# Kernel optimization log

Hardware: AMD Instinct MI355X
Metric: run time of the kernel (lower is better)

## Reference

```python
import jax, jax.numpy as jnp
import numpy as np


def setup_inputs() -> dict:
    key = jax.random.key(0)
    k1, k2, k3, k4 = jax.random.split(key, 4)
    N, C, T, V = 32, 64, 300, 25
    x = jax.random.normal(k1, (N, C, T, V), dtype=jnp.float32)
    # xavier_uniform-like scale for W (gain=1.414), small normal for alpha/phi
    xavier_scale = 1.414 * (2.0 / (C + C)) ** 0.5
    W = jax.random.normal(k2, (C, C), dtype=jnp.float32) * xavier_scale
    alpha = jax.random.normal(k3, (C // 4, C), dtype=jnp.float32) * 0.1
    phi = jax.random.normal(k4, (C // 4, C), dtype=jnp.float32) * 0.1
    return {"x": x, "W": W, "alpha": alpha, "phi": phi, "kernel": 9, "stride": 2}


def reference(x, W, alpha, phi, kernel, stride):
    N, C, T, V = x.shape
    # [N, C, T, V] -> [N*V, T, C]
    xv = jnp.transpose(x, (0, 3, 2, 1)).reshape(N * V, T, C)
    xw = xv @ W  # [NV, T, C]
    x1 = jnp.einsum('hc,ntc->nth', alpha, xw)  # [NV, T, H]
    x2 = jnp.einsum('hc,ntc->nth', phi, xw)    # [NV, T, H]
    scores = jnp.einsum('nth,nsh->nts', x1, x2)  # [NV, T, T]
    # banded local-window mask I: row i keeps cols |i-j| <= kernel//2 (multiplicative,
    # NOT -inf masking -- faithful to the original torch.mul before softmax)
    idx = jnp.arange(T)
    band = (jnp.abs(idx[:, None] - idx[None, :]) <= kernel // 2).astype(xw.dtype)
    masked = scores * band
    # one-hot selection matmul W_sel @ masked == strided row gather at 0, stride, 2*stride, ...
    sel_rows = jnp.arange(0, T, stride)  # length ceil(T/stride)
    sel = masked[:, sel_rows, :]  # [NV, T', T]
    attn = jax.nn.softmax(sel, axis=-1)
    out = jnp.einsum('nts,nsc->ntc', attn, xw)  # [NV, T', C]
    Tp = out.shape[1]
    # [NV, T', C] -> [N, C, T', V]
    return jnp.transpose(out.reshape(N, V, Tp, C), (0, 3, 2, 1))
```

## Files before the change

kernel.cpp:

```cpp
#include <hip/hip_runtime.h>

#define NB 32
#define CC 64
#define CS 32
#define TT 300
#define VV 25
#define HH 16
#define TPOUT 150
#define KH 4
#define TC 4
#define TPG 5

#define ALD 72
#define FLD 100

typedef __attribute__((ext_vector_type(4))) float f32x4;
typedef __attribute__((ext_vector_type(8))) short bf16x8;

static __device__ __forceinline__ unsigned short f2bf(float f) {
    unsigned u = __float_as_uint(f);
    unsigned r = (u + 0x7FFFu + ((u >> 16) & 1u)) >> 16;
    return (unsigned short)r;
}
static __device__ __forceinline__ float bf2f(unsigned short h) {
    return __uint_as_float(((unsigned)h) << 16);
}
static __device__ __forceinline__ float bfLO(unsigned u) {
    return __uint_as_float(u << 16);
}
static __device__ __forceinline__ float bfHI(unsigned u) {
    return __uint_as_float(u & 0xffff0000u);
}

__global__ __launch_bounds__(256) void k0_prep(const float* __restrict__ W,
                                               const float* __restrict__ alpha,
                                               const float* __restrict__ phi,
                                               unsigned short* __restrict__ Wh,
                                               unsigned short* __restrict__ Wl,
                                               float* __restrict__ ssum) {
    const int tid = threadIdx.x;
    {
        int i = blockIdx.x * 256 + tid;
        if (i < 12800)
            reinterpret_cast<float4*>(ssum)[i] = (float4){0.f, 0.f, 0.f, 0.f};
    }
    if (blockIdx.x != 0) return;

    __shared__ float sW[64][64];
    __shared__ float sA[32][64];
    __shared__ float sWe[64][96];
    for (int i = tid; i < 1024; i += 256)
        reinterpret_cast<float4*>(&sW[0][0])[i] = reinterpret_cast<const float4*>(W)[i];
    for (int i = tid; i < 512; i += 256) {
        float4 v = (i < 256) ? reinterpret_cast<const float4*>(alpha)[i]
                             : reinterpret_cast<const float4*>(phi)[i - 256];
        reinterpret_cast<float4*>(&sA[0][0])[i] = v;
    }
    __syncthreads();
    for (int i = tid; i < 1024; i += 256) {
        int ci = i >> 4, q = i & 15;
        *reinterpret_cast<float4*>(&sWe[ci][4 * q]) =
            reinterpret_cast<const float4*>(&sW[ci][0])[q];
    }
    for (int i = tid; i < 2048; i += 256) {
        int ci = i >> 5, j = i & 31;
        const float4* a = reinterpret_cast<const float4*>(&sW[ci][0]);
        const float4* b = reinterpret_cast<const float4*>(&sA[j][0]);
        float acc = 0.f;
#pragma unroll
        for (int q = 0; q < 16; ++q) {
            float4 u = a[q], w = b[q];
            acc += u.x * w.x + u.y * w.y + u.z * w.z + u.w * w.w;
        }
        sWe[ci][64 + j] = acc;
    }
    __syncthreads();
    for (int i = tid; i < 6144; i += 256) {
        int k = i / 96, c = i - 96 * k;
        float f = sWe[k][c];
        unsigned short h = f2bf(f);
        int off = (((k >> 3) * 96) + c) * 8 + (k & 7);
        Wh[off] = h;
        Wl[off] = f2bf(f - bf2f(h));
    }
}

__global__ __launch_bounds__(512) void k1_mfma(const float* __restrict__ x,
                                               const unsigned short* __restrict__ Bh,
                                               const unsigned short* __restrict__ Bl,
                                               unsigned short* __restrict__ xwv,
                                               float* __restrict__ xws,
                                               float* __restrict__ ssum) {
    __shared__ __align__(16) char smem[40000];
    unsigned short (*sAh)[ALD] = reinterpret_cast<unsigned short(*)[ALD]>(smem);
    unsigned short (*sAl)[ALD] = reinterpret_cast<unsigned short(*)[ALD]>(smem + 18432);
    float (*sF)[FLD] = reinterpret_cast<float(*)[FLD]>(smem);

    const int n  = blockIdx.y;
    const int t0 = blockIdx.x * TC;
    const int tid = threadIdx.x;

    if (tid < 400) {
        const int cig = tid & 15, tq = tid >> 4;
        const float* xp = x + (size_t)n * CC * TT * VV + (size_t)t0 * VV + 4 * tq;
        unsigned short mh[4][4], ml[4][4];
#pragma unroll
        for (int u = 0; u < 4; ++u) {
            const int ci = cig * 4 + u;
            float4 v = *reinterpret_cast<const float4*>(&xp[(size_t)ci * TT * VV]);
            unsigned short h0 = f2bf(v.x), h1 = f2bf(v.y), h2 = f2bf(v.z), h3 = f2bf(v.w);
            mh[0][u] = h0; mh[1][u] = h1; mh[2][u] = h2; mh[3][u] = h3;
            ml[0][u] = f2bf(v.x - bf2f(h0));
            ml[1][u] = f2bf(v.y - bf2f(h1));
            ml[2][u] = f2bf(v.z - bf2f(h2));
            ml[3][u] = f2bf(v.w - bf2f(h3));
        }
#pragma unroll
        for (int i = 0; i < 4; ++i) {
            *reinterpret_cast<uint2*>(&sAh[4 * tq + i][cig * 4]) =
                *reinterpret_cast<const uint2*>(&mh[i][0]);
            *reinterpret_cast<uint2*>(&sAl[4 * tq + i][cig * 4]) =
                *reinterpret_cast<const uint2*>(&ml[i][0]);
        }
    }
    __syncthreads();

    const int w    = tid >> 6;
    const int lane = tid & 63;
    const int lm   = lane & 15;
    const int g    = lane >> 4;
    const int mc   = w * 16 + lm;

    f32x4 acc[6];
#pragma unroll
    for (int b = 0; b < 6; ++b) acc[b] = (f32x4){0.f, 0.f, 0.f, 0.f};

#pragma unroll
    for (int kh = 0; kh < 2; ++kh) {
        const int kb = kh * 32 + g * 8;
        const int kc = kb >> 3;
        bf16x8 ah = *reinterpret_cast<const bf16x8*>(&sAh[mc][kb]);
        bf16x8 al = *reinterpret_cast<const bf16x8*>(&sAl[mc][kb]);
#pragma unroll
        for (int nt = 0; nt < 6; ++nt) {
            const int nc = nt * 16 + lm;
            bf16x8 bh = *reinterpret_cast<const bf16x8*>(&Bh[(size_t)(kc * 96 + nc) * 8]);
            acc[nt] = __builtin_amdgcn_mfma_f32_16x16x32_bf16(ah, bh, acc[nt], 0, 0, 0);
            if (nt >= 4) {
                bf16x8 bl = *reinterpret_cast<const bf16x8*>(&Bl[(size_t)(kc * 96 + nc) * 8]);
                acc[nt] = __builtin_amdgcn_mfma_f32_16x16x32_bf16(ah, bl, acc[nt], 0, 0, 0);
                acc[nt] = __builtin_amdgcn_mfma_f32_16x16x32_bf16(al, bh, acc[nt], 0, 0, 0);
            }
        }
    }
    __syncthreads();

#pragma unroll
    for (int j = 0; j < 4; ++j) {
        const int row = w * 16 + g * 4 + j;
        if (row < 100) {
#pragma unroll
            for (int nt = 0; nt < 6; ++nt)
                sF[row][nt * 16 + lm] = acc[nt][j];
        }
    }
    __syncthreads();

    for (int i = tid; i < 1600; i += 512) {
        const int vv = i >> 6, c = i & 63;
        float s = sF[vv][c] + sF[vv + 25][c] + sF[vv + 50][c] + sF[vv + 75][c];
        atomicAdd(&ssum[((size_t)n * VV + vv) * CC + c], s);
    }
    for (int i = tid; i < 1600; i += 512) {
        const int row = i >> 4, q = i & 15;
        const int tloc = row / 25, vv = row - 25 * tloc;
        size_t dst = (((size_t)n * VV + vv) * TT + (t0 + tloc)) * CC + 4 * q;
        float4 v = *reinterpret_cast<const float4*>(&sF[row][4 * q]);
        ushort4 b = {f2bf(v.x), f2bf(v.y), f2bf(v.z), f2bf(v.w)};
        *reinterpret_cast<ushort4*>(&xwv[dst]) = b;
    }
    for (int i = tid; i < 800; i += 512) {
        const int row = i >> 3, q = i & 7;
        const int tloc = row / 25, vv = row - 25 * tloc;
        size_t dst = (((size_t)n * VV + vv) * TT + (t0 + tloc)) * CS + 4 * q;
        *reinterpret_cast<float4*>(&xws[dst]) =
            *reinterpret_cast<const float4*>(&sF[row][64 + 4 * q]);
    }
}

__global__ __launch_bounds__(512) void k2_fused(const unsigned short* __restrict__ xwv,
                                                const float* __restrict__ xws,
                                                const float* __restrict__ ssum,
                                                float* __restrict__ out) {
    const int tpg = blockIdx.x;
    const int n   = blockIdx.y;
    const int tid = threadIdx.x;
    const int tp0 = tpg * TPG;

    __shared__ float sOut[TPG * VV][65];
    __shared__ float sss[VV][CC];
    __shared__ float sscore[TPG][VV][9];
    __shared__ float scoef[TPG][VV][10];

    for (int i = tid; i < VV * CC; i += 512)
        (&sss[0][0])[i] = ssum[((size_t)n * VV) * CC + i];

    for (int j = tid; j < TPG * VV * 9; j += 512) {
        const int tpl = j / (VV * 9);
        const int rem = j - tpl * (VV * 9);
        const int v = rem / 9, k = rem - 9 * v;
        const int t = 2 * (tp0 + tpl);
        const int s = t - KH + k;
        float sc = 0.f;
        if (s >= 0 && s < TT) {
            const size_t r = (size_t)n * VV + v;
            const float4* x1 = reinterpret_cast<const float4*>(&xws[(r * TT + t) * CS]);
            const float4* x2 = reinterpret_cast<const float4*>(&xws[(r * TT + s) * CS + 16]);
#pragma unroll
            for (int q = 0; q < 4; ++q) {
                float4 a = x1[q], b = x2[q];
                sc += a.x * b.x + a.y * b.y + a.z * b.z + a.w * b.w;
            }
        }
        sscore[tpl][v][k] = sc;
    }
    __syncthreads();

    for (int j = tid; j < TPG * VV; j += 512) {
        const int tpl = j / VV, v = j - tpl * VV;
        const int t = 2 * (tp0 + tpl);
        float m = 0.f;
        int nb = 0;
#pragma unroll
        for (int k = 0; k < 9; ++k) {
            int s = t - KH + k;
            if (s >= 0 && s < TT) { nb++; m = fmaxf(m, sscore[tpl][v][k]); }
        }
        float wbg = __expf(-m);
        float Z = (float)(TT - nb) * wbg;
        float e[9];
#pragma unroll
        for (int k = 0; k < 9; ++k) {
            int s = t - KH + k;
            float ek = (s >= 0 && s < TT) ? __expf(sscore[tpl][v][k] - m) : 0.f;
            e[k] = ek;
            Z += ek;
        }
        float inv = 1.f / Z;
#pragma unroll
        for (int k = 0; k < 9; ++k) {
            int s = t - KH + k;
            scoef[tpl][v][k] = (s >= 0 && s < TT) ? (e[k] - wbg) * inv : 0.f;
        }
        scoef[tpl][v][9] = wbg * inv;
    }
    __syncthreads();

    for (int j = tid; j < TPG * VV * 8; j += 512) {
        const int w  = j >> 3;
        const int cg = j & 7;
        const int tpl = w / VV, v = w - tpl * VV;
        const int t = 2 * (tp0 + tpl);
        const size_t rbase = ((size_t)n * VV + v) * TT;
        const int c0 = cg * 8;

        float val[8];
        {
            const float cbg = scoef[tpl][v][9];
#pragma unroll
            for (int i = 0; i < 8; ++i) val[i] = cbg * sss[v][c0 + i];
        }
#pragma unroll
        for (int k = 0; k < 9; ++k) {
            int s = t - KH + k;
            s = min(max(s, 0), TT - 1);
            const float cf = scoef[tpl][v][k];
            uint4 u = *reinterpret_cast<const uint4*>(&xwv[(rbase + s) * CC + c0]);
            val[0] = fmaf(cf, bfLO(u.x), val[0]);
            val[1] = fmaf(cf, bfHI(u.x), val[1]);
            val[2] = fmaf(cf, bfLO(u.y), val[2]);
            val[3] = fmaf(cf, bfHI(u.y), val[3]);
            val[4] = fmaf(cf, bfLO(u.z), val[4]);
            val[5] = fmaf(cf, bfHI(u.z), val[5]);
            val[6] = fmaf(cf, bfLO(u.w), val[6]);
            val[7] = fmaf(cf, bfHI(u.w), val[7]);
        }
#pragma unroll
        for (int i = 0; i < 8; ++i) sOut[w][c0 + i] = val[i];
    }
    __syncthreads();

    float* dst = out + ((size_t)n * CC * TPOUT * VV + (size_t)tp0 * VV);
    for (int j = tid; j < CC * TPG * VV; j += 512) {
        const int c = j / (TPG * VV);
        const int w = j - c * (TPG * VV);
        dst[(size_t)c * (TPOUT * VV) + w] = sOut[w][c];
    }
}

extern "C" void kernel_launch(void* const* d_in, const int* in_sizes, int n_in,
                              void* d_out, int out_size, void* d_ws, size_t ws_size,
                              hipStream_t stream) {
    const float* x     = (const float*)d_in[0];
    const float* W     = (const float*)d_in[1];
    const float* alpha = (const float*)d_in[2];
    const float* phi   = (const float*)d_in[3];
    float* out = (float*)d_out;

    float* xws  = (float*)d_ws;
    float* ssum = xws + (size_t)800 * 300 * CS;
    unsigned short* xwv = (unsigned short*)(ssum + (size_t)800 * 64);
    unsigned short* Wh  = xwv + (size_t)800 * 300 * CC;
    unsigned short* Wl  = Wh + 6144;

    k0_prep<<<64, 256, 0, stream>>>(W, alpha, phi, Wh, Wl, ssum);
    dim3 g1(TT / TC, NB);
    k1_mfma<<<g1, 512, 0, stream>>>(x, Wh, Wl, xwv, xws, ssum);
    dim3 g2(TPOUT / TPG, NB);
    k2_fused<<<g2, 512, 0, stream>>>(xwv, xws, ssum, out);
}
```

Before: 72.22 us.

## Process three time chunks per k1 block with deferred register-held stores

Each k1 block now loops over three consecutive time chunks instead of one, cutting the grid by a factor of three. It issues the next chunk's global loads of x before writing back the previous chunk's results, which are held in registers. The aim is to overlap global load latency with the write-back and atomic traffic, and to spread launch and setup cost over more work. In exchange it uses more registers and an extra barrier per iteration, and the grid shrinks to 25x32 blocks, which may underfill the GPU.

```diff
diff --git a/kernel.cpp b/kernel.cpp
--- a/kernel.cpp
+++ b/kernel.cpp
@@ -9,6 +9,7 @@
 #define TPOUT 150
 #define KH 4
 #define TC 4
+#define TPB 3
 #define TPG 5
 
 #define ALD 72
@@ -97,94 +98,196 @@
     float (*sF)[FLD] = reinterpret_cast<float(*)[FLD]>(smem);
 
     const int n  = blockIdx.y;
-    const int t0 = blockIdx.x * TC;
+    const int tg = blockIdx.x;
     const int tid = threadIdx.x;
-
-    if (tid < 400) {
-        const int cig = tid & 15, tq = tid >> 4;
-        const float* xp = x + (size_t)n * CC * TT * VV + (size_t)t0 * VV + 4 * tq;
-        unsigned short mh[4][4], ml[4][4];
-#pragma unroll
-        for (int u = 0; u < 4; ++u) {
-            const int ci = cig * 4 + u;
-            float4 v = *reinterpret_cast<const float4*>(&xp[(size_t)ci * TT * VV]);
-            unsigned short h0 = f2bf(v.x), h1 = f2bf(v.y), h2 = f2bf(v.z), h3 = f2bf(v.w);
-            mh[0][u] = h0; mh[1][u] = h1; mh[2][u] = h2; mh[3][u] = h3;
-            ml[0][u] = f2bf(v.x - bf2f(h0));
-            ml[1][u] = f2bf(v.y - bf2f(h1));
-            ml[2][u] = f2bf(v.z - bf2f(h2));
-            ml[3][u] = f2bf(v.w - bf2f(h3));
-        }
-#pragma unroll
-        for (int i = 0; i < 4; ++i) {
-            *reinterpret_cast<uint2*>(&sAh[4 * tq + i][cig * 4]) =
-                *reinterpret_cast<const uint2*>(&mh[i][0]);
-            *reinterpret_cast<uint2*>(&sAl[4 * tq + i][cig * 4]) =
-                *reinterpret_cast<const uint2*>(&ml[i][0]);
-        }
-    }
-    __syncthreads();
-
     const int w    = tid >> 6;
     const int lane = tid & 63;
     const int lm   = lane & 15;
     const int g    = lane >> 4;
     const int mc   = w * 16 + lm;
-
-    f32x4 acc[6];
-#pragma unroll
-    for (int b = 0; b < 6; ++b) acc[b] = (f32x4){0.f, 0.f, 0.f, 0.f};
-
-#pragma unroll
-    for (int kh = 0; kh < 2; ++kh) {
-        const int kb = kh * 32 + g * 8;
-        const int kc = kb >> 3;
-        bf16x8 ah = *reinterpret_cast<const bf16x8*>(&sAh[mc][kb]);
-        bf16x8 al = *reinterpret_cast<const bf16x8*>(&sAl[mc][kb]);
-#pragma unroll
-        for (int nt = 0; nt < 6; ++nt) {
-            const int nc = nt * 16 + lm;
-            bf16x8 bh = *reinterpret_cast<const bf16x8*>(&Bh[(size_t)(kc * 96 + nc) * 8]);
-            acc[nt] = __builtin_amdgcn_mfma_f32_16x16x32_bf16(ah, bh, acc[nt], 0, 0, 0);
-            if (nt >= 4) {
-                bf16x8 bl = *reinterpret_cast<const bf16x8*>(&Bl[(size_t)(kc * 96 + nc) * 8]);
-                acc[nt] = __builtin_amdgcn_mfma_f32_16x16x32_bf16(ah, bl, acc[nt], 0, 0, 0);
-                acc[nt] = __builtin_amdgcn_mfma_f32_16x16x32_bf16(al, bh, acc[nt], 0, 0, 0);
-            }
-        }
-    }
-    __syncthreads();
-
-#pragma unroll
-    for (int j = 0; j < 4; ++j) {
-        const int row = w * 16 + g * 4 + j;
-        if (row < 100) {
-#pragma unroll
-            for (int nt = 0; nt < 6; ++nt)
-                sF[row][nt * 16 + lm] = acc[nt][j];
-        }
-    }
-    __syncthreads();
-
-    for (int i = tid; i < 1600; i += 512) {
-        const int vv = i >> 6, c = i & 63;
-        float s = sF[vv][c] + sF[vv + 25][c] + sF[vv + 50][c] + sF[vv + 75][c];
-        atomicAdd(&ssum[((size_t)n * VV + vv) * CC + c], s);
-    }
-    for (int i = tid; i < 1600; i += 512) {
-        const int row = i >> 4, q = i & 15;
-        const int tloc = row / 25, vv = row - 25 * tloc;
-        size_t dst = (((size_t)n * VV + vv) * TT + (t0 + tloc)) * CC + 4 * q;
-        float4 v = *reinterpret_cast<const float4*>(&sF[row][4 * q]);
-        ushort4 b = {f2bf(v.x), f2bf(v.y), f2bf(v.z), f2bf(v.w)};
-        *reinterpret_cast<ushort4*>(&xwv[dst]) = b;
-    }
-    for (int i = tid; i < 800; i += 512) {
-        const int row = i >> 3, q = i & 7;
-        const int tloc = row / 25, vv = row - 25 * tloc;
-        size_t dst = (((size_t)n * VV + vv) * TT + (t0 + tloc)) * CS + 4 * q;
-        *reinterpret_cast<float4*>(&xws[dst]) =
-            *reinterpret_cast<const float4*>(&sF[row][64 + 4 * q]);
+    const int cig = tid & 15, tq = tid >> 4;
+
+    ushort4 xv0 = {}, xv1 = {}, xv2 = {}, xv3 = {};
+    float4  xs0 = {}, xs1 = {};
+    float   cs0 = 0.f, cs1 = 0.f, cs2 = 0.f, cs3 = 0.f;
+
+#pragma unroll
+    for (int it = 0; it < TPB; ++it) {
+        const int t0 = (tg * TPB + it) * TC;
+
+        float4 ld0, ld1, ld2, ld3;
+        if (tid < 400) {
+            const float* xp = x + (size_t)n * CC * TT * VV + (size_t)t0 * VV + 4 * tq;
+            ld0 = *reinterpret_cast<const float4*>(&xp[(size_t)(cig * 4 + 0) * TT * VV]);
+            ld1 = *reinterpret_cast<const float4*>(&xp[(size_t)(cig * 4 + 1) * TT * VV]);
+            ld2 = *reinterpret_cast<const float4*>(&xp[(size_t)(cig * 4 + 2) * TT * VV]);
+            ld3 = *reinterpret_cast<const float4*>(&xp[(size_t)(cig * 4 + 3) * TT * VV]);
+        }
+
+        if (it > 0) {
+            const int pt0 = (tg * TPB + it - 1) * TC;
+            {
+                int i = tid;
+                int row = i >> 4, q = i & 15, tloc = row / 25, vv = row - 25 * tloc;
+                *reinterpret_cast<ushort4*>(&xwv[(((size_t)n * VV + vv) * TT + pt0 + tloc) * CC + 4 * q]) = xv0;
+                i = tid + 512;
+                row = i >> 4; q = i & 15; tloc = row / 25; vv = row - 25 * tloc;
+                *reinterpret_cast<ushort4*>(&xwv[(((size_t)n * VV + vv) * TT + pt0 + tloc) * CC + 4 * q]) = xv1;
+                i = tid + 1024;
+                row = i >> 4; q = i & 15; tloc = row / 25; vv = row - 25 * tloc;
+                *reinterpret_cast<ushort4*>(&xwv[(((size_t)n * VV + vv) * TT + pt0 + tloc) * CC + 4 * q]) = xv2;
+                if (tid < 64) {
+                    i = tid + 1536;
+                    row = i >> 4; q = i & 15; tloc = row / 25; vv = row - 25 * tloc;
+                    *reinterpret_cast<ushort4*>(&xwv[(((size_t)n * VV + vv) * TT + pt0 + tloc) * CC + 4 * q]) = xv3;
+                }
+            }
+            {
+                int i = tid;
+                int row = i >> 3, q = i & 7, tloc = row / 25, vv = row - 25 * tloc;
+                *reinterpret_cast<float4*>(&xws[(((size_t)n * VV + vv) * TT + pt0 + tloc) * CS + 4 * q]) = xs0;
+                if (tid < 288) {
+                    i = tid + 512;
+                    row = i >> 3; q = i & 7; tloc = row / 25; vv = row - 25 * tloc;
+                    *reinterpret_cast<float4*>(&xws[(((size_t)n * VV + vv) * TT + pt0 + tloc) * CS + 4 * q]) = xs1;
+                }
+            }
+            {
+                const int c = tid & 63;
+                atomicAdd(&ssum[((size_t)n * VV + (tid >> 6)) * CC + c], cs0);
+                atomicAdd(&ssum[((size_t)n * VV + (tid >> 6) + 8) * CC + c], cs1);
+                atomicAdd(&ssum[((size_t)n * VV + (tid >> 6) + 16) * CC + c], cs2);
+                if (tid < 64) atomicAdd(&ssum[((size_t)n * VV + 24) * CC + tid], cs3);
+            }
+        }
+
+        if (tid < 400) {
+            unsigned short mh[4][4], ml[4][4];
+            float4 lds[4] = {ld0, ld1, ld2, ld3};
+#pragma unroll
+            for (int u = 0; u < 4; ++u) {
+                float4 v = lds[u];
+                unsigned short h0 = f2bf(v.x), h1 = f2bf(v.y), h2 = f2bf(v.z), h3 = f2bf(v.w);
+                mh[0][u] = h0; mh[1][u] = h1; mh[2][u] = h2; mh[3][u] = h3;
+                ml[0][u] = f2bf(v.x - bf2f(h0));
+                ml[1][u] = f2bf(v.y - bf2f(h1));
+                ml[2][u] = f2bf(v.z - bf2f(h2));
+                ml[3][u] = f2bf(v.w - bf2f(h3));
+            }
+#pragma unroll
+            for (int i = 0; i < 4; ++i) {
+                *reinterpret_cast<uint2*>(&sAh[4 * tq + i][cig * 4]) =
+                    *reinterpret_cast<const uint2*>(&mh[i][0]);
+                *reinterpret_cast<uint2*>(&sAl[4 * tq + i][cig * 4]) =
+                    *reinterpret_cast<const uint2*>(&ml[i][0]);
+            }
+        }
+        __syncthreads();
+
+        f32x4 acc[6];
+#pragma unroll
+        for (int b = 0; b < 6; ++b) acc[b] = (f32x4){0.f, 0.f, 0.f, 0.f};
+#pragma unroll
+        for (int kh = 0; kh < 2; ++kh) {
+            const int kb = kh * 32 + g * 8;
+            const int kc = kb >> 3;
+            bf16x8 ah = *reinterpret_cast<const bf16x8*>(&sAh[mc][kb]);
+            bf16x8 al = *reinterpret_cast<const bf16x8*>(&sAl[mc][kb]);
+#pragma unroll
+            for (int nt = 0; nt < 6; ++nt) {
+                const int nc = nt * 16 + lm;
+                bf16x8 bh = *reinterpret_cast<const bf16x8*>(&Bh[(size_t)(kc * 96 + nc) * 8]);
+                acc[nt] = __builtin_amdgcn_mfma_f32_16x16x32_bf16(ah, bh, acc[nt], 0, 0, 0);
+                if (nt >= 4) {
+                    bf16x8 bl = *reinterpret_cast<const bf16x8*>(&Bl[(size_t)(kc * 96 + nc) * 8]);
+                    acc[nt] = __builtin_amdgcn_mfma_f32_16x16x32_bf16(ah, bl, acc[nt], 0, 0, 0);
+                    acc[nt] = __builtin_amdgcn_mfma_f32_16x16x32_bf16(al, bh, acc[nt], 0, 0, 0);
+                }
+            }
+        }
+        __syncthreads();
+
+#pragma unroll
+        for (int j = 0; j < 4; ++j) {
+            const int row = w * 16 + g * 4 + j;
+            if (row < 100) {
+#pragma unroll
+                for (int nt = 0; nt < 6; ++nt)
+                    sF[row][nt * 16 + lm] = acc[nt][j];
+            }
+        }
+        __syncthreads();
+
+        {
+            const int c = tid & 63;
+            const int v0 = tid >> 6;
+            cs0 = sF[v0][c]      + sF[v0 + 25][c]      + sF[v0 + 50][c]      + sF[v0 + 75][c];
+            cs1 = sF[v0 + 8][c]  + sF[v0 + 33][c]      + sF[v0 + 58][c]      + sF[v0 + 83][c];
+            cs2 = sF[v0 + 16][c] + sF[v0 + 41][c]      + sF[v0 + 66][c]      + sF[v0 + 91][c];
+            if (tid < 64)
+                cs3 = sF[24][c] + sF[49][c] + sF[74][c] + sF[99][c];
+        }
+        {
+            int i = tid;
+            float4 v = *reinterpret_cast<const float4*>(&sF[i >> 4][4 * (i & 15)]);
+            xv0 = (ushort4){f2bf(v.x), f2bf(v.y), f2bf(v.z), f2bf(v.w)};
+            i = tid + 512;
+            v = *reinterpret_cast<const float4*>(&sF[i >> 4][4 * (i & 15)]);
+            xv1 = (ushort4){f2bf(v.x), f2bf(v.y), f2bf(v.z), f2bf(v.w)};
+            i = tid + 1024;
+            v = *reinterpret_cast<const float4*>(&sF[i >> 4][4 * (i & 15)]);
+            xv2 = (ushort4){f2bf(v.x), f2bf(v.y), f2bf(v.z), f2bf(v.w)};
+            if (tid < 64) {
+                i = tid + 1536;
+                v = *reinterpret_cast<const float4*>(&sF[i >> 4][4 * (i & 15)]);
+                xv3 = (ushort4){f2bf(v.x), f2bf(v.y), f2bf(v.z), f2bf(v.w)};
+            }
+        }
+        {
+            xs0 = *reinterpret_cast<const float4*>(&sF[tid >> 3][64 + 4 * (tid & 7)]);
+            if (tid < 288) {
+                int i = tid + 512;
+                xs1 = *reinterpret_cast<const float4*>(&sF[i >> 3][64 + 4 * (i & 7)]);
+            }
+        }
+        __syncthreads();
+    }
+
+    {
+        const int pt0 = (tg * TPB + TPB - 1) * TC;
+        {
+            int i = tid;
+            int row = i >> 4, q = i & 15, tloc = row / 25, vv = row - 25 * tloc;
+            *reinterpret_cast<ushort4*>(&xwv[(((size_t)n * VV + vv) * TT + pt0 + tloc) * CC + 4 * q]) = xv0;
+            i = tid + 512;
+            row = i >> 4; q = i & 15; tloc = row / 25; vv = row - 25 * tloc;
+            *reinterpret_cast<ushort4*>(&xwv[(((size_t)n * VV + vv) * TT + pt0 + tloc) * CC + 4 * q]) = xv1;
+            i = tid + 1024;
+            row = i >> 4; q = i & 15; tloc = row / 25; vv = row - 25 * tloc;
+            *reinterpret_cast<ushort4*>(&xwv[(((size_t)n * VV + vv) * TT + pt0 + tloc) * CC + 4 * q]) = xv2;
+            if (tid < 64) {
+                i = tid + 1536;
+                row = i >> 4; q = i & 15; tloc = row / 25; vv = row - 25 * tloc;
+                *reinterpret_cast<ushort4*>(&xwv[(((size_t)n * VV + vv) * TT + pt0 + tloc) * CC + 4 * q]) = xv3;
+            }
+        }
+        {
+            int i = tid;
+            int row = i >> 3, q = i & 7, tloc = row / 25, vv = row - 25 * tloc;
+            *reinterpret_cast<float4*>(&xws[(((size_t)n * VV + vv) * TT + pt0 + tloc) * CS + 4 * q]) = xs0;
+            if (tid < 288) {
+                i = tid + 512;
+                row = i >> 3; q = i & 7; tloc = row / 25; vv = row - 25 * tloc;
+                *reinterpret_cast<float4*>(&xws[(((size_t)n * VV + vv) * TT + pt0 + tloc) * CS + 4 * q]) = xs1;
+            }
+        }
+        {
+            const int c = tid & 63;
+            atomicAdd(&ssum[((size_t)n * VV + (tid >> 6)) * CC + c], cs0);
+            atomicAdd(&ssum[((size_t)n * VV + (tid >> 6) + 8) * CC + c], cs1);
+            atomicAdd(&ssum[((size_t)n * VV + (tid >> 6) + 16) * CC + c], cs2);
+            if (tid < 64) atomicAdd(&ssum[((size_t)n * VV + 24) * CC + tid], cs3);
+        }
     }
 }
 
@@ -314,7 +417,7 @@
     unsigned short* Wl  = Wh + 6144;
 
     k0_prep<<<64, 256, 0, stream>>>(W, alpha, phi, Wh, Wl, ssum);
-    dim3 g1(TT / TC, NB);
+    dim3 g1(TT / (TC * TPB), NB);
     k1_mfma<<<g1, 512, 0, stream>>>(x, Wh, Wl, xwv, xws, ssum);
     dim3 g2(TPOUT / TPG, NB);
     k2_fused<<<g2, 512, 0, stream>>>(xwv, xws, ssum, out);
```

New measurement: 85.96 us. 1.19x slower.
